# Kernel optimization log

Hardware: AMD Instinct MI355X
Metric: run time of the kernel (lower is better)

## Reference

```python
import jax, jax.numpy as jnp
import numpy as np

B, T, I, H = 64, 4096, 128, 128


def setup_inputs() -> dict:
    key = jax.random.key(0)
    k1, k2 = jax.random.split(key)
    X = jax.random.normal(k1, (B, T, I), dtype=jnp.float32)
    # matches torch init: randn(I+H, H) / sqrt(I+H), bias zeros
    weight = jax.random.normal(k2, (I + H, H), dtype=jnp.float32) / np.float32(np.sqrt(I + H))
    bias = jnp.zeros((H,), dtype=jnp.float32)
    return {"X": X, "weight": weight, "bias": bias}


def reference(X, weight, bias):
    # X: [B, T, I]; weight: [I+H, H]; bias: [H]
    in_size = X.shape[-1]
    W_x = weight[:in_size]   # [I, H]
    W_h = weight[in_size:]   # [H, H]
    hsz = weight.shape[1]

    def step(h, x_t):
        # h: [B, H], x_t: [B, I]  (whole batch per timestep, fused)
        h_new = jnp.tanh(x_t @ W_x + h @ W_h + bias)
        return h_new, h_new

    h0 = jnp.zeros((X.shape[0], hsz), dtype=X.dtype)
    _, hs = jax.lax.scan(step, h0, jnp.swapaxes(X, 0, 1))  # hs: [T, B, H]
    out = jnp.swapaxes(hs, 0, 1)  # [B, T, H]
    # original returns (h, h[-1:, :, :]) -- slice of last BATCH element
    return out, out[-1:, :, :]
```

## Files before the change

kernel.cpp:

```cpp
#include <hip/hip_runtime.h>
#include <stdint.h>

typedef float f32x4 __attribute__((ext_vector_type(4)));
typedef short s16x8 __attribute__((ext_vector_type(8)));

#define TLEN 4096
#define HID  128
#define NG   4

static __device__ __forceinline__ float asf(uint32_t u) {
    union { uint32_t u; float f; } v; v.u = u; return v.f;
}
static __device__ __forceinline__ uint32_t cvtpk(float lo, float hi) {
    uint32_t r;
    asm("v_cvt_pk_bf16_f32 %0, %1, %2" : "=v"(r) : "v"(lo), "v"(hi));
    return r;
}
static __device__ __forceinline__ float tanh_fast(float x) {
    return 1.f - 2.f * __builtin_amdgcn_rcpf(1.f + __builtin_amdgcn_exp2f(2.8853900817779268f * x));
}
static __device__ __forceinline__ void splitbf(float v, unsigned short& hi, unsigned short& lo) {
    uint32_t p = cvtpk(v, 0.f);
    hi = (unsigned short)(p & 0xFFFFu);
    float r = v - asf((uint32_t)hi << 16);
    uint32_t q = cvtpk(r, 0.f);
    lo = (unsigned short)(q & 0xFFFFu);
}


__global__ __launch_bounds__(512) void pre_gemm(
        const float* __restrict__ X, const float* __restrict__ W,
        const float* __restrict__ bias, float* preB,
        size_t SG, size_t SW, size_t SH, size_t ST) {
    const int tid = threadIdx.x;
    const int w  = tid >> 6;
    const int l  = tid & 63;
    const int lg = l >> 4;
    const int lc = l & 15;
    const int g  = blockIdx.x & (NG - 1);
    const int t0 = (blockIdx.x >> 2) << 4;

    s16x8 ahi[4], alo[4];
#pragma unroll
    for (int kk = 0; kk < 4; ++kk) {
        union { s16x8 v; unsigned short u[8]; } Ah, Al;
#pragma unroll
        for (int j = 0; j < 8; ++j) {
            const int k = 32*kk + 8*lg + j;
            splitbf(W[k*HID + 16*w + lc], Ah.u[j], Al.u[j]);
        }
        ahi[kk] = Ah.v; alo[kk] = Al.v;
    }
    f32x4 cb;
    {
        const float4 bv = *(const float4*)(bias + 16*w + 4*lg);
        cb[0] = bv.x; cb[1] = bv.y; cb[2] = bv.z; cb[3] = bv.w;
    }
    const int b = g*16 + lc;
    const float* xp = X + ((size_t)b*TLEN + t0)*HID + 8*lg;
    float* pp = preB + (size_t)g*SG + (size_t)w*SW + (size_t)(l>>5)*SH
                     + (size_t)t0*ST + (size_t)(l&31)*4;

    for (int tt = 0; tt < 16; ++tt) {
        f32x4 c1 = cb;
        f32x4 c2 = {0.f,0.f,0.f,0.f};
        f32x4 c3 = {0.f,0.f,0.f,0.f};
#pragma unroll
        for (int kk = 0; kk < 4; ++kk) {
            const float4 f0 = *(const float4*)(xp + 32*kk);
            const float4 f1 = *(const float4*)(xp + 32*kk + 4);
            const uint32_t p01 = cvtpk(f0.x, f0.y), p23 = cvtpk(f0.z, f0.w);
            const uint32_t p45 = cvtpk(f1.x, f1.y), p67 = cvtpk(f1.z, f1.w);
            const float r0 = f0.x - asf(p01 << 16), r1 = f0.y - asf(p01 & 0xFFFF0000u);
            const float r2 = f0.z - asf(p23 << 16), r3 = f0.w - asf(p23 & 0xFFFF0000u);
            const float r4 = f1.x - asf(p45 << 16), r5 = f1.y - asf(p45 & 0xFFFF0000u);
            const float r6 = f1.z - asf(p67 << 16), r7 = f1.w - asf(p67 & 0xFFFF0000u);
            union { s16x8 v; uint32_t u[4]; } BH, BL;
            BH.u[0] = p01; BH.u[1] = p23; BH.u[2] = p45; BH.u[3] = p67;
            BL.u[0] = cvtpk(r0, r1); BL.u[1] = cvtpk(r2, r3);
            BL.u[2] = cvtpk(r4, r5); BL.u[3] = cvtpk(r6, r7);
            c1 = __builtin_amdgcn_mfma_f32_16x16x32_bf16(ahi[kk], BH.v, c1, 0, 0, 0);
            c2 = __builtin_amdgcn_mfma_f32_16x16x32_bf16(ahi[kk], BL.v, c2, 0, 0, 0);
            c3 = __builtin_amdgcn_mfma_f32_16x16x32_bf16(alo[kk], BH.v, c3, 0, 0, 0);
        }
        f32x4 c;
        c[0] = c1[0]+c2[0]+c3[0]; c[1] = c1[1]+c2[1]+c3[1];
        c[2] = c1[2]+c2[2]+c3[2]; c[3] = c1[3]+c2[3]+c3[3];
        *(f32x4*)pp = c;
        pp += ST;
        xp += HID;
    }
}

__global__ __launch_bounds__(512) void rnn_rec(
        const float* preB, const float* __restrict__ W, float* out,
        size_t SG, size_t SW, size_t SH, size_t ST) {
    const int tid = threadIdx.x;
    const int w  = tid >> 6;
    const int l  = tid & 63;
    const int lg = l >> 4;
    const int lc = l & 15;
    const int g  = blockIdx.x;

    __shared__ uint4 lds4[1024];
    char* hb = (char*)lds4;
    {
        uint32_t* z = (uint32_t*)hb;
#pragma unroll
        for (int p = 0; p < 8; ++p) z[tid + 512*p] = 0u;
    }

    s16x8 ahi[4], alo[4];
#pragma unroll
    for (int kk = 0; kk < 4; ++kk) {
        union { s16x8 v; unsigned short u[8]; } Ah, Al;
#pragma unroll
        for (int j = 0; j < 8; ++j) {
            const int k = 32*kk + 8*lg + j;
            splitbf(W[(HID + k)*HID + 16*w + lc], Ah.u[j], Al.u[j]);
        }
        ahi[kk] = Ah.v; alo[kk] = Al.v;
    }

    const int mask = (lc & 7) << 4;
    const int rd0 = lc*256 + ((  0 + 16*lg) ^ mask);
    const int rd1 = lc*256 + (( 64 + 16*lg) ^ mask);
    const int rd2 = lc*256 + ((128 + 16*lg) ^ mask);
    const int rd3 = lc*256 + ((192 + 16*lg) ^ mask);
    const int wro = lc*256 + ((32*w + 8*lg) ^ mask);

    const float* ppf = preB + (size_t)g*SG + (size_t)w*SW + (size_t)(l>>5)*SH
                            + (size_t)(l&31)*4;
    float* op  = out + ((size_t)(g*16 + lc)*TLEN)*HID + 16*w + 4*lg;
    float* op2 = out + (size_t)64*TLEN*HID + 16*w + 4*lg;
    const bool last = (g == NG-1) && (lc == 15);

    f32x4 pf[8];
#pragma unroll
    for (int d = 0; d < 8; ++d) pf[d] = *(const f32x4*)(ppf + (size_t)d*ST);

    __syncthreads();

    for (int tb = 0; tb < TLEN; tb += 8) {
#pragma unroll
        for (int u = 0; u < 8; ++u) {
            const int t = tb + u;
            int tn = t + 8; if (tn > TLEN-1) tn = TLEN-1;
            const f32x4 nf = *(const f32x4*)(ppf + (size_t)tn*ST);

            const char* rb_ = hb + ((u & 1) ? 4096 : 0);
            char*       wb_ = hb + ((u & 1) ? 0    : 4096);

            const s16x8 bh0 = *(const s16x8*)(rb_ + rd0);
            const s16x8 bh1 = *(const s16x8*)(rb_ + rd1);
            const s16x8 bh2 = *(const s16x8*)(rb_ + rd2);
            const s16x8 bh3 = *(const s16x8*)(rb_ + rd3);
            const s16x8 bl0 = *(const s16x8*)(rb_ + 8192 + rd0);
            const s16x8 bl1 = *(const s16x8*)(rb_ + 8192 + rd1);
            const s16x8 bl2 = *(const s16x8*)(rb_ + 8192 + rd2);
            const s16x8 bl3 = *(const s16x8*)(rb_ + 8192 + rd3);

            f32x4 c1 = pf[u]; pf[u] = nf;
            f32x4 c2 = {0.f,0.f,0.f,0.f};
            f32x4 c3 = {0.f,0.f,0.f,0.f};
            c1 = __builtin_amdgcn_mfma_f32_16x16x32_bf16(ahi[0], bh0, c1, 0, 0, 0);
            c1 = __builtin_amdgcn_mfma_f32_16x16x32_bf16(ahi[1], bh1, c1, 0, 0, 0);
            c1 = __builtin_amdgcn_mfma_f32_16x16x32_bf16(ahi[2], bh2, c1, 0, 0, 0);
            c1 = __builtin_amdgcn_mfma_f32_16x16x32_bf16(ahi[3], bh3, c1, 0, 0, 0);
            c2 = __builtin_amdgcn_mfma_f32_16x16x32_bf16(ahi[0], bl0, c2, 0, 0, 0);
            c2 = __builtin_amdgcn_mfma_f32_16x16x32_bf16(ahi[1], bl1, c2, 0, 0, 0);
            c2 = __builtin_amdgcn_mfma_f32_16x16x32_bf16(ahi[2], bl2, c2, 0, 0, 0);
            c2 = __builtin_amdgcn_mfma_f32_16x16x32_bf16(ahi[3], bl3, c2, 0, 0, 0);
            c3 = __builtin_amdgcn_mfma_f32_16x16x32_bf16(alo[0], bh0, c3, 0, 0, 0);
            c3 = __builtin_amdgcn_mfma_f32_16x16x32_bf16(alo[1], bh1, c3, 0, 0, 0);
            c3 = __builtin_amdgcn_mfma_f32_16x16x32_bf16(alo[2], bh2, c3, 0, 0, 0);
            c3 = __builtin_amdgcn_mfma_f32_16x16x32_bf16(alo[3], bh3, c3, 0, 0, 0);

            const float h0 = tanh_fast(c1[0]+c2[0]+c3[0]);
            const float h1 = tanh_fast(c1[1]+c2[1]+c3[1]);
            const float h2 = tanh_fast(c1[2]+c2[2]+c3[2]);
            const float h3 = tanh_fast(c1[3]+c2[3]+c3[3]);

            float4 hv; hv.x = h0; hv.y = h1; hv.z = h2; hv.w = h3;
            *(float4*)(op + (size_t)t*HID) = hv;
            if (last) *(float4*)(op2 + (size_t)t*HID) = hv;

            const uint32_t x01 = cvtpk(h0, h1), x23 = cvtpk(h2, h3);
            const float l0 = h0 - asf(x01 << 16), l1 = h1 - asf(x01 & 0xFFFF0000u);
            const float l2 = h2 - asf(x23 << 16), l3 = h3 - asf(x23 & 0xFFFF0000u);
            uint2 wh; wh.x = x01; wh.y = x23;
            uint2 wl; wl.x = cvtpk(l0, l1); wl.y = cvtpk(l2, l3);
            *(uint2*)(wb_ + wro) = wh;
            *(uint2*)(wb_ + 8192 + wro) = wl;

            __syncthreads();
        }
    }
}

extern "C" void kernel_launch(void* const* d_in, const int* in_sizes, int n_in,
                              void* d_out, int out_size, void* d_ws, size_t ws_size,
                              hipStream_t stream) {
    const float* X    = (const float*)d_in[0];
    const float* Wt   = (const float*)d_in[1];
    const float* bias = (const float*)d_in[2];
    float* out = (float*)d_out;

    const size_t need = (size_t)NG * TLEN * 2048 * sizeof(float);
    float* preB;
    size_t SG, SW, SH, ST;
    if (ws_size >= need) {
        preB = (float*)d_ws;
        SG = (size_t)TLEN * 2048; SW = 256; SH = 128; ST = 2048;
    } else {
        preB = out;
        SG = (size_t)16 * TLEN * HID; SW = (size_t)2 * TLEN * HID;
        SH = (size_t)TLEN * HID;      ST = HID;
    }

    pre_gemm<<<dim3(NG * 256), dim3(512), 0, stream>>>(X, Wt, bias, preB, SG, SW, SH, ST);
    rnn_rec <<<dim3(NG),       dim3(512), 0, stream>>>(preB, Wt, out, SG, SW, SH, ST);
}
```

Before: 2.358 ms.

## Use 4 waves per RNN block with 32 hidden units each and register reuse

The recurrent kernel now runs 4 waves of 256 threads instead of 8, with each wave computing 32 hidden columns (two MFMA tiles), so fewer waves meet at each per-step barrier. Each wave keeps its own slice of h in registers and reads only the other waves' slices from LDS, using a new swizzled layout. The tanh scale constant is folded into W and the bias ahead of time. The barrier is replaced with a raw lgkmcnt wait plus s_barrier, and the preactivation layout is reworked to match. In exchange each wave does twice the MFMA work per step on the serial critical path.

```diff
diff --git a/kernel.cpp b/kernel.cpp
--- a/kernel.cpp
+++ b/kernel.cpp
@@ -7,6 +7,7 @@
 #define TLEN 4096
 #define HID  128
 #define NG   4
+#define KSCALE 2.8853900817779268f
 
 static __device__ __forceinline__ float asf(uint32_t u) {
     union { uint32_t u; float f; } v; v.u = u; return v.f;
@@ -15,9 +16,6 @@
     uint32_t r;
     asm("v_cvt_pk_bf16_f32 %0, %1, %2" : "=v"(r) : "v"(lo), "v"(hi));
     return r;
-}
-static __device__ __forceinline__ float tanh_fast(float x) {
-    return 1.f - 2.f * __builtin_amdgcn_rcpf(1.f + __builtin_amdgcn_exp2f(2.8853900817779268f * x));
 }
 static __device__ __forceinline__ void splitbf(float v, unsigned short& hi, unsigned short& lo) {
     uint32_t p = cvtpk(v, 0.f);
@@ -30,8 +28,7 @@
 
 __global__ __launch_bounds__(512) void pre_gemm(
         const float* __restrict__ X, const float* __restrict__ W,
-        const float* __restrict__ bias, float* preB,
-        size_t SG, size_t SW, size_t SH, size_t ST) {
+        const float* __restrict__ bias, float* preB, int wsOK) {
     const int tid = threadIdx.x;
     const int w  = tid >> 6;
     const int l  = tid & 63;
@@ -40,6 +37,10 @@
     const int g  = blockIdx.x & (NG - 1);
     const int t0 = (blockIdx.x >> 2) << 4;
 
+    const int wv = w >> 1, dd = w & 1;
+    const int GA = 32*wv + 4*dd + 8*(lc>>2) + (lc&3);
+    const int Gc = 32*wv + 4*dd + 8*lg;
+
     s16x8 ahi[4], alo[4];
 #pragma unroll
     for (int kk = 0; kk < 4; ++kk) {
@@ -47,19 +48,21 @@
 #pragma unroll
         for (int j = 0; j < 8; ++j) {
             const int k = 32*kk + 8*lg + j;
-            splitbf(W[k*HID + 16*w + lc], Ah.u[j], Al.u[j]);
+            splitbf(W[k*HID + GA] * KSCALE, Ah.u[j], Al.u[j]);
         }
         ahi[kk] = Ah.v; alo[kk] = Al.v;
     }
     f32x4 cb;
     {
-        const float4 bv = *(const float4*)(bias + 16*w + 4*lg);
-        cb[0] = bv.x; cb[1] = bv.y; cb[2] = bv.z; cb[3] = bv.w;
+        const float4 bv = *(const float4*)(bias + Gc);
+        cb[0] = bv.x*KSCALE; cb[1] = bv.y*KSCALE;
+        cb[2] = bv.z*KSCALE; cb[3] = bv.w*KSCALE;
     }
     const int b = g*16 + lc;
     const float* xp = X + ((size_t)b*TLEN + t0)*HID + 8*lg;
-    float* pp = preB + (size_t)g*SG + (size_t)w*SW + (size_t)(l>>5)*SH
-                     + (size_t)t0*ST + (size_t)(l&31)*4;
+    float* pp; size_t ST;
+    if (wsOK) { pp = preB + ((size_t)g*TLEN + t0)*2048 + w*256 + l*4; ST = 2048; }
+    else      { pp = preB + ((size_t)b*TLEN + t0)*HID + Gc;           ST = HID;  }
 
     for (int tt = 0; tt < 16; ++tt) {
         f32x4 c1 = cb;
@@ -92,108 +95,146 @@
     }
 }
 
-__global__ __launch_bounds__(512) void rnn_rec(
-        const float* preB, const float* __restrict__ W, float* out,
-        size_t SG, size_t SW, size_t SH, size_t ST) {
+template<int WS>
+__global__ __launch_bounds__(256) void rnn_rec(
+        const float* preB, const float* __restrict__ W, float* out) {
     const int tid = threadIdx.x;
-    const int w  = tid >> 6;
-    const int l  = tid & 63;
-    const int lg = l >> 4;
-    const int lc = l & 15;
-    const int g  = blockIdx.x;
-
-    __shared__ uint4 lds4[1024];
-    char* hb = (char*)lds4;
+    const int l   = tid & 63;
+    const int lg  = l >> 4;
+    const int lc  = l & 15;
+    const int g   = blockIdx.x;
+    const int wvu = __builtin_amdgcn_readfirstlane(tid >> 6);
+
+    __shared__ uint4 ldsb[1024];
+    char* hb = (char*)ldsb;
     {
-        uint32_t* z = (uint32_t*)hb;
-#pragma unroll
-        for (int p = 0; p < 8; ++p) z[tid + 512*p] = 0u;
-    }
-
-    s16x8 ahi[4], alo[4];
-#pragma unroll
-    for (int kk = 0; kk < 4; ++kk) {
-        union { s16x8 v; unsigned short u[8]; } Ah, Al;
-#pragma unroll
-        for (int j = 0; j < 8; ++j) {
-            const int k = 32*kk + 8*lg + j;
-            splitbf(W[(HID + k)*HID + 16*w + lc], Ah.u[j], Al.u[j]);
-        }
-        ahi[kk] = Ah.v; alo[kk] = Al.v;
-    }
-
-    const int mask = (lc & 7) << 4;
-    const int rd0 = lc*256 + ((  0 + 16*lg) ^ mask);
-    const int rd1 = lc*256 + (( 64 + 16*lg) ^ mask);
-    const int rd2 = lc*256 + ((128 + 16*lg) ^ mask);
-    const int rd3 = lc*256 + ((192 + 16*lg) ^ mask);
-    const int wro = lc*256 + ((32*w + 8*lg) ^ mask);
-
-    const float* ppf = preB + (size_t)g*SG + (size_t)w*SW + (size_t)(l>>5)*SH
-                            + (size_t)(l&31)*4;
-    float* op  = out + ((size_t)(g*16 + lc)*TLEN)*HID + 16*w + 4*lg;
-    float* op2 = out + (size_t)64*TLEN*HID + 16*w + 4*lg;
-    const bool last = (g == NG-1) && (lc == 15);
-
-    f32x4 pf[8];
-#pragma unroll
-    for (int d = 0; d < 8; ++d) pf[d] = *(const f32x4*)(ppf + (size_t)d*ST);
+        uint32_t* z = (uint32_t*)ldsb;
+#pragma unroll
+        for (int p = 0; p < 16; ++p) z[tid + 256*p] = 0u;
+    }
+
+    s16x8 ahi[2][4], alo[2][4];
+#pragma unroll
+    for (int d = 0; d < 2; ++d) {
+        const int GAd = 32*wvu + 4*d + 8*(lc>>2) + (lc&3);
+#pragma unroll
+        for (int kk = 0; kk < 4; ++kk) {
+            union { s16x8 v; unsigned short u[8]; } Ah, Al;
+#pragma unroll
+            for (int j = 0; j < 8; ++j) {
+                const int k = 32*kk + 8*lg + j;
+                splitbf(W[(size_t)(HID + k)*HID + GAd] * KSCALE, Ah.u[j], Al.u[j]);
+            }
+            ahi[d][kk] = Ah.v; alo[d][kk] = Al.v;
+        }
+    }
+
+    const int swz = ((l >> 3) << 7) + ((((l & 7) ^ ((l >> 3) & 7))) << 4);
+
+    const float* pb; int PST, od;
+    if (WS) { pb = preB + (size_t)g*TLEN*2048 + wvu*512 + l*4;            PST = 2048; od = 256; }
+    else    { pb = preB + ((size_t)(g*16+lc)*TLEN)*HID + 32*wvu + 8*lg;   PST = HID;  od = 4;   }
+
+    float* po  = out + ((size_t)(g*16+lc)*TLEN)*HID + 32*wvu + 8*lg;
+    float* po2 = out + (size_t)64*TLEN*HID + 32*wvu + 8*lg;
+    const bool lastb = (g == NG-1) && (lc == 15);
+
+    f32x4 pf[4][2];
+#pragma unroll
+    for (int u = 0; u < 4; ++u) {
+        pf[u][0] = *(const f32x4*)(pb + (size_t)u*PST);
+        pf[u][1] = *(const f32x4*)(pb + (size_t)u*PST + od);
+    }
+
+    s16x8 bh_own = {0,0,0,0,0,0,0,0};
+    s16x8 bl_own = {0,0,0,0,0,0,0,0};
 
     __syncthreads();
 
-    for (int tb = 0; tb < TLEN; tb += 8) {
-#pragma unroll
-        for (int u = 0; u < 8; ++u) {
-            const int t = tb + u;
-            int tn = t + 8; if (tn > TLEN-1) tn = TLEN-1;
-            const f32x4 nf = *(const f32x4*)(ppf + (size_t)tn*ST);
-
-            const char* rb_ = hb + ((u & 1) ? 4096 : 0);
-            char*       wb_ = hb + ((u & 1) ? 0    : 4096);
-
-            const s16x8 bh0 = *(const s16x8*)(rb_ + rd0);
-            const s16x8 bh1 = *(const s16x8*)(rb_ + rd1);
-            const s16x8 bh2 = *(const s16x8*)(rb_ + rd2);
-            const s16x8 bh3 = *(const s16x8*)(rb_ + rd3);
-            const s16x8 bl0 = *(const s16x8*)(rb_ + 8192 + rd0);
-            const s16x8 bl1 = *(const s16x8*)(rb_ + 8192 + rd1);
-            const s16x8 bl2 = *(const s16x8*)(rb_ + 8192 + rd2);
-            const s16x8 bl3 = *(const s16x8*)(rb_ + 8192 + rd3);
-
-            f32x4 c1 = pf[u]; pf[u] = nf;
-            f32x4 c2 = {0.f,0.f,0.f,0.f};
-            f32x4 c3 = {0.f,0.f,0.f,0.f};
-            c1 = __builtin_amdgcn_mfma_f32_16x16x32_bf16(ahi[0], bh0, c1, 0, 0, 0);
-            c1 = __builtin_amdgcn_mfma_f32_16x16x32_bf16(ahi[1], bh1, c1, 0, 0, 0);
-            c1 = __builtin_amdgcn_mfma_f32_16x16x32_bf16(ahi[2], bh2, c1, 0, 0, 0);
-            c1 = __builtin_amdgcn_mfma_f32_16x16x32_bf16(ahi[3], bh3, c1, 0, 0, 0);
-            c2 = __builtin_amdgcn_mfma_f32_16x16x32_bf16(ahi[0], bl0, c2, 0, 0, 0);
-            c2 = __builtin_amdgcn_mfma_f32_16x16x32_bf16(ahi[1], bl1, c2, 0, 0, 0);
-            c2 = __builtin_amdgcn_mfma_f32_16x16x32_bf16(ahi[2], bl2, c2, 0, 0, 0);
-            c2 = __builtin_amdgcn_mfma_f32_16x16x32_bf16(ahi[3], bl3, c2, 0, 0, 0);
-            c3 = __builtin_amdgcn_mfma_f32_16x16x32_bf16(alo[0], bh0, c3, 0, 0, 0);
-            c3 = __builtin_amdgcn_mfma_f32_16x16x32_bf16(alo[1], bh1, c3, 0, 0, 0);
-            c3 = __builtin_amdgcn_mfma_f32_16x16x32_bf16(alo[2], bh2, c3, 0, 0, 0);
-            c3 = __builtin_amdgcn_mfma_f32_16x16x32_bf16(alo[3], bh3, c3, 0, 0, 0);
-
-            const float h0 = tanh_fast(c1[0]+c2[0]+c3[0]);
-            const float h1 = tanh_fast(c1[1]+c2[1]+c3[1]);
-            const float h2 = tanh_fast(c1[2]+c2[2]+c3[2]);
-            const float h3 = tanh_fast(c1[3]+c2[3]+c3[3]);
-
-            float4 hv; hv.x = h0; hv.y = h1; hv.z = h2; hv.w = h3;
-            *(float4*)(op + (size_t)t*HID) = hv;
-            if (last) *(float4*)(op2 + (size_t)t*HID) = hv;
-
-            const uint32_t x01 = cvtpk(h0, h1), x23 = cvtpk(h2, h3);
-            const float l0 = h0 - asf(x01 << 16), l1 = h1 - asf(x01 & 0xFFFF0000u);
-            const float l2 = h2 - asf(x23 << 16), l3 = h3 - asf(x23 & 0xFFFF0000u);
-            uint2 wh; wh.x = x01; wh.y = x23;
-            uint2 wl; wl.x = cvtpk(l0, l1); wl.y = cvtpk(l2, l3);
-            *(uint2*)(wb_ + wro) = wh;
-            *(uint2*)(wb_ + 8192 + wro) = wl;
-
-            __syncthreads();
+    for (int tb = 0; tb < TLEN; tb += 4) {
+#pragma unroll
+        for (int u = 0; u < 4; ++u) {
+            const int t   = tb + u;
+            const int par = u & 1;
+            const char* rb = hb + (par ^ 1) * 8192;
+            char*       wb = hb + par * 8192;
+
+#define LDCH(K, BH_, BL_) \
+            s16x8 BH_, BL_; \
+            if (K != wvu) { \
+                BH_ = *(const s16x8*)(rb + (K)*2048 + swz); \
+                BL_ = *(const s16x8*)(rb + (K)*2048 + 1024 + swz); \
+            } else { BH_ = bh_own; BL_ = bl_own; }
+            LDCH(0, bh0, bl0)
+            LDCH(1, bh1, bl1)
+            LDCH(2, bh2, bl2)
+            LDCH(3, bh3, bl3)
+#undef LDCH
+
+            f32x4 c1[2], c2[2], c3[2];
+            c1[0] = pf[u][0]; c1[1] = pf[u][1];
+            c2[0] = f32x4{0.f,0.f,0.f,0.f}; c2[1] = f32x4{0.f,0.f,0.f,0.f};
+            c3[0] = f32x4{0.f,0.f,0.f,0.f}; c3[1] = f32x4{0.f,0.f,0.f,0.f};
+
+            if (t + 4 < TLEN) {
+                pf[u][0] = *(const f32x4*)(pb + (size_t)(t+4)*PST);
+                pf[u][1] = *(const f32x4*)(pb + (size_t)(t+4)*PST + od);
+            }
+
+#define MSTEP(K, BH_, BL_) \
+            c1[0] = __builtin_amdgcn_mfma_f32_16x16x32_bf16(ahi[0][K], BH_, c1[0], 0,0,0); \
+            c1[1] = __builtin_amdgcn_mfma_f32_16x16x32_bf16(ahi[1][K], BH_, c1[1], 0,0,0); \
+            c2[0] = __builtin_amdgcn_mfma_f32_16x16x32_bf16(ahi[0][K], BL_, c2[0], 0,0,0); \
+            c2[1] = __builtin_amdgcn_mfma_f32_16x16x32_bf16(ahi[1][K], BL_, c2[1], 0,0,0); \
+            c3[0] = __builtin_amdgcn_mfma_f32_16x16x32_bf16(alo[0][K], BH_, c3[0], 0,0,0); \
+            c3[1] = __builtin_amdgcn_mfma_f32_16x16x32_bf16(alo[1][K], BH_, c3[1], 0,0,0);
+            MSTEP(0, bh0, bl0)
+            MSTEP(1, bh1, bl1)
+            MSTEP(2, bh2, bl2)
+            MSTEP(3, bh3, bl3)
+#undef MSTEP
+
+            float hh[2][4];
+#pragma unroll
+            for (int d = 0; d < 2; ++d)
+#pragma unroll
+                for (int j = 0; j < 4; ++j) {
+                    const float s = c1[d][j] + c2[d][j] + c3[d][j];
+                    hh[d][j] = 1.f - 2.f * __builtin_amdgcn_rcpf(1.f + __builtin_amdgcn_exp2f(s));
+                }
+
+            float4 hv0, hv1;
+            hv0.x = hh[0][0]; hv0.y = hh[0][1]; hv0.z = hh[0][2]; hv0.w = hh[0][3];
+            hv1.x = hh[1][0]; hv1.y = hh[1][1]; hv1.z = hh[1][2]; hv1.w = hh[1][3];
+            *(float4*)(po + (size_t)t*HID)     = hv0;
+            *(float4*)(po + (size_t)t*HID + 4) = hv1;
+            if (lastb) {
+                *(float4*)(po2 + (size_t)t*HID)     = hv0;
+                *(float4*)(po2 + (size_t)t*HID + 4) = hv1;
+            }
+
+            union { s16x8 v; uint4 q4; uint32_t q[4]; } BH, BL;
+#pragma unroll
+            for (int d = 0; d < 2; ++d) {
+                const uint32_t xa = cvtpk(hh[d][0], hh[d][1]);
+                const uint32_t xb = cvtpk(hh[d][2], hh[d][3]);
+                const float r0 = hh[d][0] - asf(xa << 16);
+                const float r1 = hh[d][1] - asf(xa & 0xFFFF0000u);
+                const float r2 = hh[d][2] - asf(xb << 16);
+                const float r3 = hh[d][3] - asf(xb & 0xFFFF0000u);
+                BH.q[2*d]   = xa;            BH.q[2*d+1] = xb;
+                BL.q[2*d]   = cvtpk(r0, r1); BL.q[2*d+1] = cvtpk(r2, r3);
+            }
+            bh_own = BH.v; bl_own = BL.v;
+            *(uint4*)(wb + wvu*2048 + swz)        = BH.q4;
+            *(uint4*)(wb + wvu*2048 + 1024 + swz) = BL.q4;
+
+            if (WS) {
+                asm volatile("s_waitcnt lgkmcnt(0)\n\ts_barrier" ::: "memory");
+                __builtin_amdgcn_sched_barrier(0);
+            } else {
+                __syncthreads();
+            }
         }
     }
 }
@@ -207,17 +248,12 @@
     float* out = (float*)d_out;
 
     const size_t need = (size_t)NG * TLEN * 2048 * sizeof(float);
-    float* preB;
-    size_t SG, SW, SH, ST;
     if (ws_size >= need) {
-        preB = (float*)d_ws;
-        SG = (size_t)TLEN * 2048; SW = 256; SH = 128; ST = 2048;
+        float* preB = (float*)d_ws;
+        pre_gemm<<<dim3(NG * 256), dim3(512), 0, stream>>>(X, Wt, bias, preB, 1);
+        rnn_rec<1><<<dim3(NG), dim3(256), 0, stream>>>(preB, Wt, out);
     } else {
-        preB = out;
-        SG = (size_t)16 * TLEN * HID; SW = (size_t)2 * TLEN * HID;
-        SH = (size_t)TLEN * HID;      ST = HID;
-    }
-
-    pre_gemm<<<dim3(NG * 256), dim3(512), 0, stream>>>(X, Wt, bias, preB, SG, SW, SH, ST);
-    rnn_rec <<<dim3(NG),       dim3(512), 0, stream>>>(preB, Wt, out, SG, SW, SH, ST);
-}
+        pre_gemm<<<dim3(NG * 256), dim3(512), 0, stream>>>(X, Wt, bias, out, 0);
+        rnn_rec<0><<<dim3(NG), dim3(256), 0, stream>>>(out, Wt, out);
+    }
+}
```

New measurement: 4.326 ms. +83.5%, slower.
